# Kernel optimization log

Hardware: AMD Instinct MI355X
Metric: run time of the kernel (lower is better)

## Reference

```python
import jax, jax.numpy as jnp
import numpy as np

V = 32000; D = 1024; H = 16; L = 2; T = 2048; B = 4; C = 32000
DH = D // H
EPS = 1e-5


def layernorm(x, g, b):
    mu = jnp.mean(x, axis=-1, keepdims=True)
    var = jnp.mean((x - mu) ** 2, axis=-1, keepdims=True)
    return (x - mu) * jax.lax.rsqrt(var + EPS) * g + b


def setup_inputs() -> dict:
    key = jax.random.key(0)
    ks = jax.random.split(key, 16)
    s = 0.02
    return {
        "tokens": jax.random.randint(ks[0], (B, T), 0, V),
        "embed_W": jax.random.normal(ks[1], (V, D), jnp.float32) * s,
        "pos_W": jax.random.normal(ks[2], (T, D), jnp.float32) * s,
        "ln_g": jnp.ones((L, D), jnp.float32),
        "ln_b": jnp.zeros((L, D), jnp.float32),
        "qkv_W": jax.random.normal(ks[3], (L, D, 3 * D), jnp.float32) * s,
        "qkv_b": jnp.zeros((L, 3 * D), jnp.float32),
        "out_W": jax.random.normal(ks[4], (L, D, D), jnp.float32) * s,
        "out_b": jnp.zeros((L, D), jnp.float32),
        "lnf_g": jnp.ones((D,), jnp.float32),
        "lnf_b": jnp.zeros((D,), jnp.float32),
        "head_W": jax.random.normal(ks[5], (D, C), jnp.float32) * s,
        "head_b": jnp.zeros((C,), jnp.float32),
    }


def attn_block(x, g, b, Wqkv, bqkv, Wo, bo):
    # pre-LN attention + residual. NOTE: original module defines an MLP but never calls it.
    h = layernorm(x, g, b)
    qkv = h @ Wqkv + bqkv                      # [B,T,3D]
    q, k, v = jnp.split(qkv, 3, axis=-1)
    q = q.reshape(B, T, H, DH)
    k = k.reshape(B, T, H, DH)
    v = v.reshape(B, T, H, DH)
    scores = jnp.einsum("bqhd,bkhd->bhqk", q, k) / np.sqrt(DH)
    causal = jnp.tril(jnp.ones((T, T), bool))
    scores = jnp.where(causal, scores, -jnp.inf)
    attn = jax.nn.softmax(scores, axis=-1)
    o = jnp.einsum("bhqk,bkhd->bqhd", attn, v).reshape(B, T, D)
    return x + o @ Wo + bo


def reference(tokens, embed_W, pos_W, ln_g, ln_b, qkv_W, qkv_b, out_W, out_b,
              lnf_g, lnf_b, head_W, head_b):
    h = embed_W[tokens] + pos_W[jnp.arange(T)][None, :, :]   # [B,T,D]
    for i in range(L):
        h = attn_block(h, ln_g[i], ln_b[i], qkv_W[i], qkv_b[i], out_W[i], out_b[i])
    h = layernorm(h, lnf_g, lnf_b)
    logits = h[:, -1] @ head_W + head_b                      # [B,C]
    return logits
```

## Files before the change

### kernel.cpp

```cpp
#include <hip/hip_runtime.h>

typedef __attribute__((ext_vector_type(8))) __bf16 bf16x8;
typedef __attribute__((ext_vector_type(4))) __bf16 bf16x4;
typedef __attribute__((ext_vector_type(4))) float f32x4;
typedef unsigned long long ull;

static constexpr int kB = 4, kT = 2048, kD = 1024, kH = 16;
static constexpr int kC = 32000, kM = 8192, k3D = 3072, kQK = 2048;

#define MFMA16(a, b, c) __builtin_amdgcn_mfma_f32_16x16x32_bf16((a), (b), (c), 0, 0, 0)

__device__ __forceinline__ void gload_lds16(const __bf16* g, __bf16* l) {
  __builtin_amdgcn_global_load_lds(
      (const __attribute__((address_space(1))) unsigned int*)(const void*)g,
      (__attribute__((address_space(3))) unsigned int*)(void*)l, 16, 0, 0);
}

__global__ __launch_bounds__(256) void embed_ln_kernel(const int* __restrict__ tok,
                                                       const float* __restrict__ embW,
                                                       const float* __restrict__ posW,
                                                       const float* __restrict__ g,
                                                       const float* __restrict__ bb,
                                                       float* __restrict__ h,
                                                       __bf16* __restrict__ hn) {
  const int row = blockIdx.x, tid = threadIdx.x;
  const int t = row & (kT - 1);
  const int tk = tok[row];
  const f32x4 e = ((const f32x4*)(embW + (size_t)tk * kD))[tid];
  const f32x4 p = ((const f32x4*)(posW + (size_t)t * kD))[tid];
  const f32x4 xv = e + p;
  ((f32x4*)(h + (size_t)row * kD))[tid] = xv;
  float s  = xv[0] + xv[1] + xv[2] + xv[3];
  float s2 = xv[0]*xv[0] + xv[1]*xv[1] + xv[2]*xv[2] + xv[3]*xv[3];
  #pragma unroll
  for (int off = 1; off < 64; off <<= 1) {
    s  += __shfl_xor(s, off);
    s2 += __shfl_xor(s2, off);
  }
  __shared__ float red[8];
  const int w = tid >> 6;
  if ((tid & 63) == 0) { red[w*2] = s; red[w*2+1] = s2; }
  __syncthreads();
  s  = red[0] + red[2] + red[4] + red[6];
  s2 = red[1] + red[3] + red[5] + red[7];
  const float mu  = s * (1.f / kD);
  const float var = s2 * (1.f / kD) - mu * mu;
  const float rs  = rsqrtf(var + 1e-5f);
  const f32x4 gv = ((const f32x4*)g)[tid];
  const f32x4 bv = ((const f32x4*)bb)[tid];
  bf16x4 o;
  #pragma unroll
  for (int i = 0; i < 4; i++) o[i] = (__bf16)((xv[i] - mu) * rs * gv[i] + bv[i]);
  ((bf16x4*)(hn + (size_t)row * kD))[tid] = o;
}

template <bool BF16OUT>
__global__ __launch_bounds__(256) void ln_kernel(const float* __restrict__ x,
                                                 const float* __restrict__ g,
                                                 const float* __restrict__ bb,
                                                 void* __restrict__ outp) {
  const int row = blockIdx.x, tid = threadIdx.x;
  const f32x4 xv = ((const f32x4*)(x + (size_t)row * kD))[tid];
  float s  = xv[0] + xv[1] + xv[2] + xv[3];
  float s2 = xv[0]*xv[0] + xv[1]*xv[1] + xv[2]*xv[2] + xv[3]*xv[3];
  #pragma unroll
  for (int off = 1; off < 64; off <<= 1) {
    s  += __shfl_xor(s, off);
    s2 += __shfl_xor(s2, off);
  }
  __shared__ float red[8];
  const int w = tid >> 6;
  if ((tid & 63) == 0) { red[w*2] = s; red[w*2+1] = s2; }
  __syncthreads();
  s  = red[0] + red[2] + red[4] + red[6];
  s2 = red[1] + red[3] + red[5] + red[7];
  const float mu  = s * (1.f / kD);
  const float var = s2 * (1.f / kD) - mu * mu;
  const float rs  = rsqrtf(var + 1e-5f);
  const f32x4 gv = ((const f32x4*)g)[tid];
  const f32x4 bv = ((const f32x4*)bb)[tid];
  if constexpr (BF16OUT) {
    bf16x4 o;
    #pragma unroll
    for (int i = 0; i < 4; i++) o[i] = (__bf16)((xv[i] - mu) * rs * gv[i] + bv[i]);
    ((bf16x4*)((__bf16*)outp + (size_t)row * kD))[tid] = o;
  } else {
    f32x4 o;
    #pragma unroll
    for (int i = 0; i < 4; i++) o[i] = (xv[i] - mu) * rs * gv[i] + bv[i];
    ((f32x4*)((float*)outp + (size_t)row * kD))[tid] = o;
  }
}

__global__ __launch_bounds__(256) void transpose_all_kernel(const float* __restrict__ qkv_W,
                                                            const float* __restrict__ out_W,
                                                            __bf16* __restrict__ WqkvT,
                                                            __bf16* __restrict__ WoT) {
  __shared__ float sh[32][33];
  const int bid = blockIdx.x;
  const float* W; __bf16* WT; int N, tile;
  if (bid < 3072)      { W = qkv_W;                   WT = WqkvT;                    N = k3D; tile = bid; }
  else if (bid < 6144) { W = qkv_W + (size_t)kD*k3D;  WT = WqkvT + (size_t)k3D*kD;   N = k3D; tile = bid - 3072; }
  else                 { W = out_W;                   WT = WoT;                      N = kD;  tile = bid - 6144; }
  const int tx = threadIdx.x & 31, ty = threadIdx.x >> 5;
  const int ntile = N >> 5;
  const int c0 = (tile % ntile) << 5;
  const int r0 = (tile / ntile) << 5;
  #pragma unroll
  for (int i = 0; i < 4; i++) {
    const int r = ty + i * 8;
    sh[r][tx] = W[(size_t)(r0 + r) * N + c0 + tx];
  }
  __syncthreads();
  #pragma unroll
  for (int i = 0; i < 4; i++) {
    const int cc = ty + i * 8;
    WT[(size_t)(c0 + cc) * kD + r0 + tx] = (__bf16)sh[tx][cc];
  }
}

template <bool OUT_BF16>
__global__ __launch_bounds__(256) void gemm_bt_kernel(const __bf16* __restrict__ A,
                                                      const __bf16* __restrict__ BT,
                                                      const float* __restrict__ bias,
                                                      const float* resid,
                                                      float* outf,
                                                      __bf16* outb,
                                                      __bf16* vtp,
                                                      int N, int K, int ldc, int vt_c0,
                                                      int bm_mult, int bm_add) {
  __shared__ __bf16 As[128 * 64];
  __shared__ __bf16 Bs[128 * 64];
  const int tid = threadIdx.x;
  const int lane = tid & 63, w = tid >> 6;
  int wg = (int)blockIdx.x;
  const int nwg = gridDim.x;
  wg = (wg & 7) * (nwg >> 3) + (wg >> 3);
  const int nbn = N >> 7;
  const int bm = (wg / nbn) * bm_mult + bm_add;
  const int bn = wg % nbn;
  const int wr = (w >> 1) * 64, wc = (w & 1) * 64;
  const int lrow = lane & 15, lk8 = (lane >> 4) * 8;

  const int srow = lane >> 3;
  const int scol = (lane & 7) * 8;
  const __bf16* gA = A + (size_t)(bm * 128) * K;
  const __bf16* gB = BT + (size_t)(bn * 128) * K;

  f32x4 acc[4][4] = {};

  for (int k0 = 0; k0 < K; k0 += 64) {
    __syncthreads();
    #pragma unroll
    for (int i = 0; i < 4; i++) {
      const int c = w * 4 + i;
      const int row = c * 8 + srow;
      gload_lds16(gA + (size_t)row * K + k0 + scol, As + c * 512);
      gload_lds16(gB + (size_t)row * K + k0 + scol, Bs + c * 512);
    }
    __syncthreads();
    #pragma unroll
    for (int ks = 0; ks < 2; ks++) {
      bf16x8 af[4], bf[4];
      #pragma unroll
      for (int mt = 0; mt < 4; mt++)
        af[mt] = *(const bf16x8*)(As + (wr + mt * 16 + lrow) * 64 + ks * 32 + lk8);
      #pragma unroll
      for (int nt = 0; nt < 4; nt++)
        bf[nt] = *(const bf16x8*)(Bs + (wc + nt * 16 + lrow) * 64 + ks * 32 + lk8);
      __builtin_amdgcn_s_setprio(1);
      #pragma unroll
      for (int mt = 0; mt < 4; mt++)
        #pragma unroll
        for (int nt = 0; nt < 4; nt++)
          acc[mt][nt] = MFMA16(af[mt], bf[nt], acc[mt][nt]);
      __builtin_amdgcn_s_setprio(0);
    }
  }

  #pragma unroll
  for (int mt = 0; mt < 4; mt++) {
    const int row0 = bm * 128 + wr + mt * 16 + (lane >> 4) * 4;
    #pragma unroll
    for (int nt = 0; nt < 4; nt++) {
      const int col = bn * 128 + wc + nt * 16 + lrow;
      const float bsv = bias[col];
      if (vtp && col >= vt_c0) {
        const int vd = col - vt_c0;
        const int bb_ = row0 >> 11, t = row0 & (kT - 1);
        bf16x4 pk;
        #pragma unroll
        for (int r = 0; r < 4; r++) pk[r] = (__bf16)(acc[mt][nt][r] + bsv);
        *(bf16x4*)(vtp + ((size_t)((bb_ << 4) + (vd >> 6)) * 64 + (vd & 63)) * kT + t) = pk;
      } else {
        #pragma unroll
        for (int r = 0; r < 4; r++) {
          const size_t idx = (size_t)(row0 + r) * ldc + col;
          const float v = acc[mt][nt][r] + bsv;
          if constexpr (OUT_BF16) {
            outb[idx] = (__bf16)v;
          } else {
            outf[idx] = v + resid[idx];
          }
        }
      }
    }
  }
}

__global__ __launch_bounds__(256) void flash0_kernel(const __bf16* __restrict__ qkv,
                                                     const __bf16* __restrict__ vtg,
                                                     __bf16* __restrict__ o) {
  constexpr float SC = 0.18033688011112042f;
  __shared__ __bf16 Ks[64 * 64];
  __shared__ __bf16 Vs[64 * 64];
  const int tid = threadIdx.x, lane = tid & 63, w = tid >> 6;
  int wg = (int)blockIdx.x;
  const int nwg = gridDim.x;
  wg = (wg & 7) * (nwg >> 3) + (wg >> 3);
  const int sub = wg & 15, bh = wg >> 4;
  const int b = bh >> 4, hh = bh & 15;
  const int g = lane >> 4, qown = lane & 15;
  const int r8 = lane >> 3;
  const int sslot = (lane & 7) ^ (r8 & 7);
  const int swz = (qown & 7) << 3;
  const size_t row0 = (size_t)b * kT;

  for (int s = 0; s < 2; s++) {
    const int qt = s ? (31 - sub) : sub;

    const __bf16* qrow = qkv + (row0 + qt * 64 + w * 16 + qown) * kQK + hh * 64;
    bf16x8 qf[2];
    #pragma unroll
    for (int ks = 0; ks < 2; ks++) {
      bf16x8 qr = *(const bf16x8*)(qrow + ks * 32 + 8 * g);
      #pragma unroll
      for (int i = 0; i < 8; i++) qf[ks][i] = (__bf16)((float)qr[i] * SC);
    }

    float m_run = -1e30f, l_run = 0.f;
    f32x4 acc[4] = {};

    for (int kt = 0; kt <= qt; kt++) {
      __syncthreads();
      #pragma unroll
      for (int j = 0; j < 2; j++) {
        const int r = w * 16 + j * 8 + r8;
        gload_lds16(qkv + (row0 + kt * 64 + r) * kQK + 1024 + hh * 64 + sslot * 8,
                    Ks + (w * 16 + j * 8) * 64);
        gload_lds16(vtg + ((size_t)bh * 64 + r) * kT + kt * 64 + sslot * 8,
                    Vs + (w * 16 + j * 8) * 64);
      }
      __syncthreads();

      f32x4 sv[4] = {};
      #pragma unroll
      for (int nt = 0; nt < 4; nt++) {
        const int kr = nt * 16 + qown;
        #pragma unroll
        for (int ks = 0; ks < 2; ks++) {
          bf16x8 kf = *(const bf16x8*)(Ks + kr * 64 + ((ks * 32 + 8 * g) ^ swz));
          sv[nt] = MFMA16(kf, qf[ks], sv[nt]);
        }
      }
      if (kt == qt) {
        #pragma unroll
        for (int nt = 0; nt < 4; nt++)
          #pragma unroll
          for (int r = 0; r < 4; r++)
            if (nt * 16 + 4 * g + r > w * 16 + qown) sv[nt][r] = -1e30f;
      }

      float mx = -1e30f;
      #pragma unroll
      for (int nt = 0; nt < 4; nt++)
        #pragma unroll
        for (int r = 0; r < 4; r++) mx = fmaxf(mx, sv[nt][r]);
      mx = fmaxf(mx, __shfl_xor(mx, 16));
      mx = fmaxf(mx, __shfl_xor(mx, 32));

      float ps = 0.f;
      ull quad[4];
      if (__all(mx - m_run <= 8.0f)) {
        #pragma unroll
        for (int nt = 0; nt < 4; nt++) {
          union { bf16x4 v; ull u; } qd;
          #pragma unroll
          for (int r = 0; r < 4; r++) {
            const float p = exp2f(sv[nt][r] - m_run);
            ps += p;
            qd.v[r] = (__bf16)p;
          }
          quad[nt] = qd.u;
        }
        ps += __shfl_xor(ps, 16);
        ps += __shfl_xor(ps, 32);
        l_run += ps;
      } else {
        const float mnew = fmaxf(m_run, mx);
        const float fsc = exp2f(m_run - mnew);
        m_run = mnew;
        #pragma unroll
        for (int nt = 0; nt < 4; nt++) {
          union { bf16x4 v; ull u; } qd;
          #pragma unroll
          for (int r = 0; r < 4; r++) {
            const float p = exp2f(sv[nt][r] - mnew);
            ps += p;
            qd.v[r] = (__bf16)p;
          }
          quad[nt] = qd.u;
        }
        ps += __shfl_xor(ps, 16);
        ps += __shfl_xor(ps, 32);
        l_run = l_run * fsc + ps;
        float fr[4];
        #pragma unroll
        for (int r = 0; r < 4; r++) fr[r] = __shfl(fsc, 20 * g + r);
        #pragma unroll
        for (int nt = 0; nt < 4; nt++)
          #pragma unroll
          for (int r = 0; r < 4; r++) acc[nt][r] *= fr[r];
      }

      bf16x8 pf[2];
      #pragma unroll
      for (int ks = 0; ks < 2; ks++) {
        const int src = (g & 1) * 32 + qown;
        const ull t0 = __shfl(quad[2 * ks],     src);
        const ull t1 = __shfl(quad[2 * ks + 1], src);
        const ull lo = (g & 2) ? t1 : t0;
        const ull t2 = __shfl(quad[2 * ks],     src + 16);
        const ull t3 = __shfl(quad[2 * ks + 1], src + 16);
        const ull hi = (g & 2) ? t3 : t2;
        union { ull u[2]; bf16x8 v; } pk;
        pk.u[0] = lo; pk.u[1] = hi;
        pf[ks] = pk.v;
      }

      #pragma unroll
      for (int nt = 0; nt < 4; nt++) {
        const int vr = nt * 16 + qown;
        #pragma unroll
        for (int ks = 0; ks < 2; ks++) {
          bf16x8 vf = *(const bf16x8*)(Vs + vr * 64 + ((ks * 32 + 8 * g) ^ swz));
          acc[nt] = MFMA16(pf[ks], vf, acc[nt]);
        }
      }
    }

    const float li = 1.f / l_run;
    float lr[4];
    #pragma unroll
    for (int r = 0; r < 4; r++) lr[r] = __shfl(li, 20 * g + r);
    #pragma unroll
    for (int r = 0; r < 4; r++) {
      const int t = qt * 64 + w * 16 + 4 * g + r;
      #pragma unroll
      for (int nt = 0; nt < 4; nt++)
        o[(row0 + t) * kD + hh * 64 + nt * 16 + qown] = (__bf16)(acc[nt][r] * lr[r]);
    }
  }
}

__global__ __launch_bounds__(256) void flash1_kernel(const __bf16* __restrict__ qkv,
                                                     const __bf16* __restrict__ vtg,
                                                     float* __restrict__ part_acc,
                                                     float* __restrict__ part_ml) {
  constexpr float SC = 0.18033688011112042f;
  __shared__ __bf16 Ks[64 * 64];
  __shared__ __bf16 Vs[64 * 64];
  const int tid = threadIdx.x, lane = tid & 63, w = tid >> 6;
  int wg = (int)blockIdx.x;
  const int nwg = gridDim.x;
  wg = (wg & 7) * (nwg >> 3) + (wg >> 3);
  const int sub = wg & 7, bh = wg >> 3;
  const int b = bh >> 4, hh = bh & 15;
  const int g = lane >> 4, qown = lane & 15;
  const int r8 = lane >> 3;
  const int sslot = (lane & 7) ^ (r8 & 7);
  const int swz = (qown & 7) << 3;
  const size_t row0 = (size_t)b * kT;
  const int qt = 31, ktlo = sub * 4, kthi = ktlo + 4;

  const __bf16* qrow = qkv + (row0 + qt * 64 + w * 16 + qown) * kQK + hh * 64;
  bf16x8 qf[2];
  #pragma unroll
  for (int ks = 0; ks < 2; ks++) {
    bf16x8 qr = *(const bf16x8*)(qrow + ks * 32 + 8 * g);
    #pragma unroll
    for (int i = 0; i < 8; i++) qf[ks][i] = (__bf16)((float)qr[i] * SC);
  }

  float m_run = -1e30f, l_run = 0.f;
  f32x4 acc[4] = {};

  for (int kt = ktlo; kt < kthi; kt++) {
    __syncthreads();
    #pragma unroll
    for (int jj = 0; jj < 2; jj++) {
      const int r = w * 16 + jj * 8 + r8;
      gload_lds16(qkv + (row0 + kt * 64 + r) * kQK + 1024 + hh * 64 + sslot * 8,
                  Ks + (w * 16 + jj * 8) * 64);
      gload_lds16(vtg + ((size_t)bh * 64 + r) * kT + kt * 64 + sslot * 8,
                  Vs + (w * 16 + jj * 8) * 64);
    }
    __syncthreads();

    f32x4 sv[4] = {};
    #pragma unroll
    for (int nt = 0; nt < 4; nt++) {
      const int kr = nt * 16 + qown;
      #pragma unroll
      for (int ks = 0; ks < 2; ks++) {
        bf16x8 kf = *(const bf16x8*)(Ks + kr * 64 + ((ks * 32 + 8 * g) ^ swz));
        sv[nt] = MFMA16(kf, qf[ks], sv[nt]);
      }
    }
    if (kt == qt) {
      #pragma unroll
      for (int nt = 0; nt < 4; nt++)
        #pragma unroll
        for (int r = 0; r < 4; r++)
          if (nt * 16 + 4 * g + r > w * 16 + qown) sv[nt][r] = -1e30f;
    }

    float mx = -1e30f;
    #pragma unroll
    for (int nt = 0; nt < 4; nt++)
      #pragma unroll
      for (int r = 0; r < 4; r++) mx = fmaxf(mx, sv[nt][r]);
    mx = fmaxf(mx, __shfl_xor(mx, 16));
    mx = fmaxf(mx, __shfl_xor(mx, 32));

    const float mnew = fmaxf(m_run, mx);
    const float fsc = exp2f(m_run - mnew);
    m_run = mnew;
    float ps = 0.f;
    ull quad[4];
    #pragma unroll
    for (int nt = 0; nt < 4; nt++) {
      union { bf16x4 v; ull u; } qd;
      #pragma unroll
      for (int r = 0; r < 4; r++) {
        const float p = exp2f(sv[nt][r] - mnew);
        ps += p;
        qd.v[r] = (__bf16)p;
      }
      quad[nt] = qd.u;
    }
    ps += __shfl_xor(ps, 16);
    ps += __shfl_xor(ps, 32);
    l_run = l_run * fsc + ps;
    float fr[4];
    #pragma unroll
    for (int r = 0; r < 4; r++) fr[r] = __shfl(fsc, 20 * g + r);
    #pragma unroll
    for (int nt = 0; nt < 4; nt++)
      #pragma unroll
      for (int r = 0; r < 4; r++) acc[nt][r] *= fr[r];

    bf16x8 pf[2];
    #pragma unroll
    for (int ks = 0; ks < 2; ks++) {
      const int src = (g & 1) * 32 + qown;
      const ull t0 = __shfl(quad[2 * ks],     src);
      const ull t1 = __shfl(quad[2 * ks + 1], src);
      const ull lo = (g & 2) ? t1 : t0;
      const ull t2 = __shfl(quad[2 * ks],     src + 16);
      const ull t3 = __shfl(quad[2 * ks + 1], src + 16);
      const ull hi = (g & 2) ? t3 : t2;
      union { ull u[2]; bf16x8 v; } pk;
      pk.u[0] = lo; pk.u[1] = hi;
      pf[ks] = pk.v;
    }

    #pragma unroll
    for (int nt = 0; nt < 4; nt++) {
      const int vr = nt * 16 + qown;
      #pragma unroll
      for (int ks = 0; ks < 2; ks++) {
        bf16x8 vf = *(const bf16x8*)(Vs + vr * 64 + ((ks * 32 + 8 * g) ^ swz));
        acc[nt] = MFMA16(pf[ks], vf, acc[nt]);
      }
    }
  }

  const int tile = bh * 8 + sub;
  #pragma unroll
  for (int r = 0; r < 4; r++) {
    const int rr = w * 16 + 4 * g + r;
    #pragma unroll
    for (int nt = 0; nt < 4; nt++)
      part_acc[(size_t)tile * 4096 + rr * 64 + nt * 16 + qown] = acc[nt][r];
  }
  if (g == 0) {
    part_ml[tile * 128 + w * 16 + qown] = m_run;
    part_ml[tile * 128 + 64 + w * 16 + qown] = l_run;
  }
}

__global__ __launch_bounds__(256) void flash_merge_kernel(const float* __restrict__ part_acc,
                                                          const float* __restrict__ part_ml,
                                                          __bf16* __restrict__ o) {
  const int bh = blockIdx.x, b = bh >> 4, hh = bh & 15;
  for (int e = threadIdx.x; e < 4096; e += 256) {
    const int row = e >> 6, d = e & 63;
    float mstar = -1e30f;
    #pragma unroll
    for (int kc = 0; kc < 8; kc++)
      mstar = fmaxf(mstar, part_ml[(bh * 8 + kc) * 128 + row]);
    float lstar = 0.f, osum = 0.f;
    #pragma unroll
    for (int kc = 0; kc < 8; kc++) {
      const float wgt = exp2f(part_ml[(bh * 8 + kc) * 128 + row] - mstar);
      lstar += wgt * part_ml[(bh * 8 + kc) * 128 + 64 + row];
      osum  += wgt * part_acc[(size_t)(bh * 8 + kc) * 4096 + e];
    }
    o[(size_t)(b * kT + 1984 + row) * kD + hh * 64 + d] = (__bf16)(osum / lstar);
  }
}

__global__ __launch_bounds__(256) void proj_last_kernel(const __bf16* __restrict__ o,
                                                        const float* __restrict__ W,
                                                        const float* __restrict__ bias,
                                                        const float* __restrict__ h,
                                                        float* __restrict__ out4) {
  const int b = blockIdx.y;
  const int j = blockIdx.x * 256 + threadIdx.x;
  __shared__ float ov[kD];
  const __bf16* orow = o + (size_t)(b * kT + kT - 1) * kD;
  for (int i = threadIdx.x; i < kD; i += 256) ov[i] = (float)orow[i];
  __syncthreads();
  float acc = 0.f;
  #pragma unroll 8
  for (int k = 0; k < kD; k++) acc = fmaf(ov[k], W[(size_t)k * kD + j], acc);
  out4[b * kD + j] = h[(size_t)(b * kT + kT - 1) * kD + j] + bias[j] + acc;
}

__global__ __launch_bounds__(256) void head_kernel(const float* __restrict__ hl,
                                                   const float* __restrict__ W,
                                                   const float* __restrict__ hb,
                                                   float* __restrict__ out) {
  const int jj = threadIdx.x & 63, ks = threadIdx.x >> 6;
  const int j = blockIdx.x * 64 + jj;
  __shared__ float sh[kB * kD];
  __shared__ float red[4][kB][64];
  for (int i = threadIdx.x; i < kB * kD; i += 256) sh[i] = hl[i];
  __syncthreads();
  float a[kB] = {};
  const int k0 = ks * 256;
  #pragma unroll 4
  for (int k = k0; k < k0 + 256; k++) {
    const float wv = W[(size_t)k * kC + j];
    #pragma unroll
    for (int bb = 0; bb < kB; bb++) a[bb] = fmaf(sh[bb * kD + k], wv, a[bb]);
  }
  #pragma unroll
  for (int bb = 0; bb < kB; bb++) red[ks][bb][jj] = a[bb];
  __syncthreads();
  if (ks == 0) {
    const float bv = hb[j];
    #pragma unroll
    for (int bb = 0; bb < kB; bb++)
      out[(size_t)bb * kC + j] = red[0][bb][jj] + red[1][bb][jj] + red[2][bb][jj] + red[3][bb][jj] + bv;
  }
}

extern "C" void kernel_launch(void* const* d_in, const int* in_sizes, int n_in,
                              void* d_out, int out_size, void* d_ws, size_t ws_size,
                              hipStream_t stream) {
  const int*   tokens = (const int*)d_in[0];
  const float* embW   = (const float*)d_in[1];
  const float* posW   = (const float*)d_in[2];
  const float* ln_g   = (const float*)d_in[3];
  const float* ln_b   = (const float*)d_in[4];
  const float* qkv_W  = (const float*)d_in[5];
  const float* qkv_b  = (const float*)d_in[6];
  const float* out_W  = (const float*)d_in[7];
  const float* out_b  = (const float*)d_in[8];
  const float* lnf_g  = (const float*)d_in[9];
  const float* lnf_b  = (const float*)d_in[10];
  const float* headW  = (const float*)d_in[11];
  const float* headb  = (const float*)d_in[12];
  float* logits = (float*)d_out;

  char* ws = (char*)d_ws;
  float*  h     = (float*)(ws);
  __bf16* hn    = (__bf16*)(ws + 33554432);
  __bf16* qkv   = (__bf16*)(ws + 50331648);
  __bf16* Vt    = (__bf16*)(ws + 83886080);
  __bf16* ob    = (__bf16*)(ws + 100663296);
  __bf16* WqkvT = (__bf16*)(ws + 117440512);
  __bf16* WoT   = (__bf16*)(ws + 130613248);
  float*  hl4   = (float*)(ws + 132710400);
  float*  hl    = (float*)(ws + 132726784);
  float* part_acc = (float*)(ws + 33554432);
  float* part_ml  = (float*)(ws + 33554432 + 8388608);

  transpose_all_kernel<<<7168, 256, 0, stream>>>(qkv_W, out_W, WqkvT, WoT);
  embed_ln_kernel<<<kM, 256, 0, stream>>>(tokens, embW, posW, ln_g, ln_b, h, hn);

  gemm_bt_kernel<true><<<(kM/128)*(k3D/128), 256, 0, stream>>>(
      hn, WqkvT, qkv_b, nullptr, nullptr, qkv, Vt, k3D, kD, kQK, 2048, 1, 0);
  flash0_kernel<<<kB*kH*16, 256, 0, stream>>>(qkv, Vt, ob);
  gemm_bt_kernel<false><<<(kM/128)*(kD/128), 256, 0, stream>>>(
      ob, WoT, out_b, h, h, nullptr, nullptr, kD, kD, kD, 1 << 30, 1, 0);

  ln_kernel<true><<<kM, 256, 0, stream>>>(h, ln_g + kD, ln_b + kD, hn);
  gemm_bt_kernel<true><<<(kM/128)*(2048/128), 256, 0, stream>>>(
      hn, WqkvT + (size_t)k3D*kD + (size_t)kD*kD, qkv_b + k3D + kD,
      nullptr, nullptr, qkv + 1024, Vt, 2048, kD, kQK, 1024, 1, 0);
  gemm_bt_kernel<true><<<kB*(kD/128), 256, 0, stream>>>(
      hn, WqkvT + (size_t)k3D*kD, qkv_b + k3D,
      nullptr, nullptr, qkv, nullptr, kD, kD, kQK, 1 << 30, 16, 15);
  flash1_kernel<<<kB*kH*8, 256, 0, stream>>>(qkv, Vt, part_acc, part_ml);
  flash_merge_kernel<<<kB*kH, 256, 0, stream>>>(part_acc, part_ml, ob);
  proj_last_kernel<<<dim3(kD/256, kB), 256, 0, stream>>>(ob, out_W + (size_t)kD*kD,
                                                         out_b + kD, h, hl4);

  ln_kernel<false><<<kB, 256, 0, stream>>>(hl4, lnf_g, lnf_b, hl);
  head_kernel<<<500, 256, 0, stream>>>(hl, headW, headb, logits);
}
```

Measured before the change: 483.1 us.

## Fuse small kernels to cut launch count across the pipeline

Merges the weight transpose and embedding+LayerNorm into one prep kernel, and the layer-1 KV and last-tile Q GEMMs into one launch. The flash merge step moves into flash1 as a last-block-done reduction using an atomic counter and thread fences. The final LayerNorm is folded into the head kernel, which each block recomputes redundantly. This trims launch and serialization overhead, at the cost of an extra memset, atomic synchronization and duplicated LayerNorm work per head block.

```diff
diff --git a/kernel.cpp b/kernel.cpp
--- a/kernel.cpp
+++ b/kernel.cpp
@@ -16,42 +16,70 @@
       (__attribute__((address_space(3))) unsigned int*)(void*)l, 16, 0, 0);
 }
 
-__global__ __launch_bounds__(256) void embed_ln_kernel(const int* __restrict__ tok,
-                                                       const float* __restrict__ embW,
-                                                       const float* __restrict__ posW,
-                                                       const float* __restrict__ g,
-                                                       const float* __restrict__ bb,
-                                                       float* __restrict__ h,
-                                                       __bf16* __restrict__ hn) {
-  const int row = blockIdx.x, tid = threadIdx.x;
-  const int t = row & (kT - 1);
-  const int tk = tok[row];
-  const f32x4 e = ((const f32x4*)(embW + (size_t)tk * kD))[tid];
-  const f32x4 p = ((const f32x4*)(posW + (size_t)t * kD))[tid];
-  const f32x4 xv = e + p;
-  ((f32x4*)(h + (size_t)row * kD))[tid] = xv;
-  float s  = xv[0] + xv[1] + xv[2] + xv[3];
-  float s2 = xv[0]*xv[0] + xv[1]*xv[1] + xv[2]*xv[2] + xv[3]*xv[3];
-  #pragma unroll
-  for (int off = 1; off < 64; off <<= 1) {
-    s  += __shfl_xor(s, off);
-    s2 += __shfl_xor(s2, off);
-  }
-  __shared__ float red[8];
-  const int w = tid >> 6;
-  if ((tid & 63) == 0) { red[w*2] = s; red[w*2+1] = s2; }
-  __syncthreads();
-  s  = red[0] + red[2] + red[4] + red[6];
-  s2 = red[1] + red[3] + red[5] + red[7];
-  const float mu  = s * (1.f / kD);
-  const float var = s2 * (1.f / kD) - mu * mu;
-  const float rs  = rsqrtf(var + 1e-5f);
-  const f32x4 gv = ((const f32x4*)g)[tid];
-  const f32x4 bv = ((const f32x4*)bb)[tid];
-  bf16x4 o;
-  #pragma unroll
-  for (int i = 0; i < 4; i++) o[i] = (__bf16)((xv[i] - mu) * rs * gv[i] + bv[i]);
-  ((bf16x4*)(hn + (size_t)row * kD))[tid] = o;
+__global__ __launch_bounds__(256) void prep_kernel(const float* __restrict__ qkv_W,
+                                                   const float* __restrict__ out_W,
+                                                   __bf16* __restrict__ WqkvT,
+                                                   __bf16* __restrict__ WoT,
+                                                   const int* __restrict__ tok,
+                                                   const float* __restrict__ embW,
+                                                   const float* __restrict__ posW,
+                                                   const float* __restrict__ g,
+                                                   const float* __restrict__ bb,
+                                                   float* __restrict__ h,
+                                                   __bf16* __restrict__ hn) {
+  const int bid = blockIdx.x, tid = threadIdx.x;
+  if (bid < 7168) {
+    __shared__ float sh[32][33];
+    const float* W; __bf16* WT; int N, tile;
+    if (bid < 3072)      { W = qkv_W;                  WT = WqkvT;                  N = k3D; tile = bid; }
+    else if (bid < 6144) { W = qkv_W + (size_t)kD*k3D; WT = WqkvT + (size_t)k3D*kD; N = k3D; tile = bid - 3072; }
+    else                 { W = out_W;                  WT = WoT;                    N = kD;  tile = bid - 6144; }
+    const int tx = tid & 31, ty = tid >> 5;
+    const int ntile = N >> 5;
+    const int c0 = (tile % ntile) << 5;
+    const int r0 = (tile / ntile) << 5;
+    #pragma unroll
+    for (int i = 0; i < 4; i++) {
+      const int r = ty + i * 8;
+      sh[r][tx] = W[(size_t)(r0 + r) * N + c0 + tx];
+    }
+    __syncthreads();
+    #pragma unroll
+    for (int i = 0; i < 4; i++) {
+      const int cc = ty + i * 8;
+      WT[(size_t)(c0 + cc) * kD + r0 + tx] = (__bf16)sh[tx][cc];
+    }
+  } else {
+    const int row = bid - 7168;
+    const int t = row & (kT - 1);
+    const int tk = tok[row];
+    const f32x4 e = ((const f32x4*)(embW + (size_t)tk * kD))[tid];
+    const f32x4 p = ((const f32x4*)(posW + (size_t)t * kD))[tid];
+    const f32x4 xv = e + p;
+    ((f32x4*)(h + (size_t)row * kD))[tid] = xv;
+    float s  = xv[0] + xv[1] + xv[2] + xv[3];
+    float s2 = xv[0]*xv[0] + xv[1]*xv[1] + xv[2]*xv[2] + xv[3]*xv[3];
+    #pragma unroll
+    for (int off = 1; off < 64; off <<= 1) {
+      s  += __shfl_xor(s, off);
+      s2 += __shfl_xor(s2, off);
+    }
+    __shared__ float red[8];
+    const int w = tid >> 6;
+    if ((tid & 63) == 0) { red[w*2] = s; red[w*2+1] = s2; }
+    __syncthreads();
+    s  = red[0] + red[2] + red[4] + red[6];
+    s2 = red[1] + red[3] + red[5] + red[7];
+    const float mu  = s * (1.f / kD);
+    const float var = s2 * (1.f / kD) - mu * mu;
+    const float rs  = rsqrtf(var + 1e-5f);
+    const f32x4 gv = ((const f32x4*)g)[tid];
+    const f32x4 bv = ((const f32x4*)bb)[tid];
+    bf16x4 o;
+    #pragma unroll
+    for (int i = 0; i < 4; i++) o[i] = (__bf16)((xv[i] - mu) * rs * gv[i] + bv[i]);
+    ((bf16x4*)(hn + (size_t)row * kD))[tid] = o;
+  }
 }
 
 template <bool BF16OUT>
@@ -92,56 +120,19 @@
   }
 }
 
-__global__ __launch_bounds__(256) void transpose_all_kernel(const float* __restrict__ qkv_W,
-                                                            const float* __restrict__ out_W,
-                                                            __bf16* __restrict__ WqkvT,
-                                                            __bf16* __restrict__ WoT) {
-  __shared__ float sh[32][33];
-  const int bid = blockIdx.x;
-  const float* W; __bf16* WT; int N, tile;
-  if (bid < 3072)      { W = qkv_W;                   WT = WqkvT;                    N = k3D; tile = bid; }
-  else if (bid < 6144) { W = qkv_W + (size_t)kD*k3D;  WT = WqkvT + (size_t)k3D*kD;   N = k3D; tile = bid - 3072; }
-  else                 { W = out_W;                   WT = WoT;                      N = kD;  tile = bid - 6144; }
-  const int tx = threadIdx.x & 31, ty = threadIdx.x >> 5;
-  const int ntile = N >> 5;
-  const int c0 = (tile % ntile) << 5;
-  const int r0 = (tile / ntile) << 5;
-  #pragma unroll
-  for (int i = 0; i < 4; i++) {
-    const int r = ty + i * 8;
-    sh[r][tx] = W[(size_t)(r0 + r) * N + c0 + tx];
-  }
-  __syncthreads();
-  #pragma unroll
-  for (int i = 0; i < 4; i++) {
-    const int cc = ty + i * 8;
-    WT[(size_t)(c0 + cc) * kD + r0 + tx] = (__bf16)sh[tx][cc];
-  }
-}
-
 template <bool OUT_BF16>
-__global__ __launch_bounds__(256) void gemm_bt_kernel(const __bf16* __restrict__ A,
-                                                      const __bf16* __restrict__ BT,
-                                                      const float* __restrict__ bias,
-                                                      const float* resid,
-                                                      float* outf,
-                                                      __bf16* outb,
-                                                      __bf16* vtp,
-                                                      int N, int K, int ldc, int vt_c0,
-                                                      int bm_mult, int bm_add) {
-  __shared__ __bf16 As[128 * 64];
-  __shared__ __bf16 Bs[128 * 64];
+__device__ __forceinline__ void gemm_body(const __bf16* __restrict__ A,
+                                          const __bf16* __restrict__ BT,
+                                          const float* __restrict__ bias,
+                                          const float* resid, float* outf,
+                                          __bf16* outb, __bf16* vtp,
+                                          int K, int ldc, int vt_c0,
+                                          int bm, int bn,
+                                          __bf16* As, __bf16* Bs) {
   const int tid = threadIdx.x;
   const int lane = tid & 63, w = tid >> 6;
-  int wg = (int)blockIdx.x;
-  const int nwg = gridDim.x;
-  wg = (wg & 7) * (nwg >> 3) + (wg >> 3);
-  const int nbn = N >> 7;
-  const int bm = (wg / nbn) * bm_mult + bm_add;
-  const int bn = wg % nbn;
   const int wr = (w >> 1) * 64, wc = (w & 1) * 64;
   const int lrow = lane & 15, lk8 = (lane >> 4) * 8;
-
   const int srow = lane >> 3;
   const int scol = (lane & 7) * 8;
   const __bf16* gA = A + (size_t)(bm * 128) * K;
@@ -205,6 +196,44 @@
         }
       }
     }
+  }
+}
+
+template <bool OUT_BF16>
+__global__ __launch_bounds__(256) void gemm_bt_kernel(const __bf16* __restrict__ A,
+                                                      const __bf16* __restrict__ BT,
+                                                      const float* __restrict__ bias,
+                                                      const float* resid,
+                                                      float* outf, __bf16* outb, __bf16* vtp,
+                                                      int N, int K, int ldc, int vt_c0) {
+  __shared__ __bf16 As[128 * 64];
+  __shared__ __bf16 Bs[128 * 64];
+  int wg = (int)blockIdx.x;
+  const int nwg = gridDim.x;
+  wg = (wg & 7) * (nwg >> 3) + (wg >> 3);
+  const int nbn = N >> 7;
+  gemm_body<OUT_BF16>(A, BT, bias, resid, outf, outb, vtp, K, ldc, vt_c0,
+                      wg / nbn, wg % nbn, As, Bs);
+}
+
+__global__ __launch_bounds__(256) void gemm_l1_kernel(const __bf16* __restrict__ hn,
+                                                      const __bf16* __restrict__ WkvT,
+                                                      const float* __restrict__ bias_kv,
+                                                      const __bf16* __restrict__ WqT,
+                                                      const float* __restrict__ bias_q,
+                                                      __bf16* __restrict__ qkv,
+                                                      __bf16* __restrict__ vtp) {
+  __shared__ __bf16 As[128 * 64];
+  __shared__ __bf16 Bs[128 * 64];
+  int wg = (int)blockIdx.x;
+  if (wg < 1024) {
+    wg = (wg & 7) * 128 + (wg >> 3);
+    gemm_body<true>(hn, WkvT, bias_kv, nullptr, nullptr, qkv + 1024, vtp,
+                    kD, kQK, 1024, wg / 16, wg % 16, As, Bs);
+  } else {
+    wg -= 1024;
+    gemm_body<true>(hn, WqT, bias_q, nullptr, nullptr, qkv, nullptr,
+                    kD, kQK, 1 << 30, (wg >> 3) * 16 + 15, wg & 7, As, Bs);
   }
 }
 
@@ -366,7 +395,9 @@
 __global__ __launch_bounds__(256) void flash1_kernel(const __bf16* __restrict__ qkv,
                                                      const __bf16* __restrict__ vtg,
                                                      float* __restrict__ part_acc,
-                                                     float* __restrict__ part_ml) {
+                                                     float* __restrict__ part_ml,
+                                                     int* __restrict__ cnt,
+                                                     __bf16* __restrict__ o) {
   constexpr float SC = 0.18033688011112042f;
   __shared__ __bf16 Ks[64 * 64];
   __shared__ __bf16 Vs[64 * 64];
@@ -498,26 +529,28 @@
     part_ml[tile * 128 + w * 16 + qown] = m_run;
     part_ml[tile * 128 + 64 + w * 16 + qown] = l_run;
   }
-}
-
-__global__ __launch_bounds__(256) void flash_merge_kernel(const float* __restrict__ part_acc,
-                                                          const float* __restrict__ part_ml,
-                                                          __bf16* __restrict__ o) {
-  const int bh = blockIdx.x, b = bh >> 4, hh = bh & 15;
-  for (int e = threadIdx.x; e < 4096; e += 256) {
-    const int row = e >> 6, d = e & 63;
-    float mstar = -1e30f;
-    #pragma unroll
-    for (int kc = 0; kc < 8; kc++)
-      mstar = fmaxf(mstar, part_ml[(bh * 8 + kc) * 128 + row]);
-    float lstar = 0.f, osum = 0.f;
-    #pragma unroll
-    for (int kc = 0; kc < 8; kc++) {
-      const float wgt = exp2f(part_ml[(bh * 8 + kc) * 128 + row] - mstar);
-      lstar += wgt * part_ml[(bh * 8 + kc) * 128 + 64 + row];
-      osum  += wgt * part_acc[(size_t)(bh * 8 + kc) * 4096 + e];
-    }
-    o[(size_t)(b * kT + 1984 + row) * kD + hh * 64 + d] = (__bf16)(osum / lstar);
+
+  __threadfence();
+  __shared__ int lastflag;
+  if (tid == 0) lastflag = (atomicAdd(&cnt[bh], 1) == 7) ? 1 : 0;
+  __syncthreads();
+  if (lastflag) {
+    __threadfence();
+    for (int e = tid; e < 4096; e += 256) {
+      const int row = e >> 6, d = e & 63;
+      float mstar = -1e30f;
+      #pragma unroll
+      for (int kc = 0; kc < 8; kc++)
+        mstar = fmaxf(mstar, part_ml[(bh * 8 + kc) * 128 + row]);
+      float lstar = 0.f, osum = 0.f;
+      #pragma unroll
+      for (int kc = 0; kc < 8; kc++) {
+        const float wgt = exp2f(part_ml[(bh * 8 + kc) * 128 + row] - mstar);
+        lstar += wgt * part_ml[(bh * 8 + kc) * 128 + 64 + row];
+        osum  += wgt * part_acc[(size_t)(bh * 8 + kc) * 4096 + e];
+      }
+      o[(size_t)(b * kT + 1984 + row) * kD + hh * 64 + d] = (__bf16)(osum / lstar);
+    }
   }
 }
 
@@ -538,32 +571,56 @@
   out4[b * kD + j] = h[(size_t)(b * kT + kT - 1) * kD + j] + bias[j] + acc;
 }
 
-__global__ __launch_bounds__(256) void head_kernel(const float* __restrict__ hl,
+__global__ __launch_bounds__(256) void head_kernel(const float* __restrict__ hl4,
+                                                   const float* __restrict__ g,
+                                                   const float* __restrict__ bb,
                                                    const float* __restrict__ W,
                                                    const float* __restrict__ hb,
                                                    float* __restrict__ out) {
-  const int jj = threadIdx.x & 63, ks = threadIdx.x >> 6;
-  const int j = blockIdx.x * 64 + jj;
   __shared__ float sh[kB * kD];
   __shared__ float red[4][kB][64];
-  for (int i = threadIdx.x; i < kB * kD; i += 256) sh[i] = hl[i];
+  const int tid = threadIdx.x;
+  const int wv = tid >> 6, ln = tid & 63;
+  {
+    const float* row = hl4 + wv * kD;
+    float vals[16];
+    float s = 0.f, s2 = 0.f;
+    #pragma unroll
+    for (int i = 0; i < 16; i++) {
+      const float v = row[i * 64 + ln];
+      vals[i] = v; s += v; s2 += v * v;
+    }
+    #pragma unroll
+    for (int off = 1; off < 64; off <<= 1) {
+      s += __shfl_xor(s, off); s2 += __shfl_xor(s2, off);
+    }
+    const float mu = s * (1.f / kD);
+    const float rs = rsqrtf(s2 * (1.f / kD) - mu * mu + 1e-5f);
+    #pragma unroll
+    for (int i = 0; i < 16; i++) {
+      const int c = i * 64 + ln;
+      sh[wv * kD + c] = (vals[i] - mu) * rs * g[c] + bb[c];
+    }
+  }
   __syncthreads();
+  const int jj = tid & 63, ks = tid >> 6;
+  const int j = blockIdx.x * 64 + jj;
   float a[kB] = {};
   const int k0 = ks * 256;
   #pragma unroll 4
   for (int k = k0; k < k0 + 256; k++) {
-    const float wv = W[(size_t)k * kC + j];
-    #pragma unroll
-    for (int bb = 0; bb < kB; bb++) a[bb] = fmaf(sh[bb * kD + k], wv, a[bb]);
+    const float wvw = W[(size_t)k * kC + j];
+    #pragma unroll
+    for (int b2 = 0; b2 < kB; b2++) a[b2] = fmaf(sh[b2 * kD + k], wvw, a[b2]);
   }
   #pragma unroll
-  for (int bb = 0; bb < kB; bb++) red[ks][bb][jj] = a[bb];
+  for (int b2 = 0; b2 < kB; b2++) red[ks][b2][jj] = a[b2];
   __syncthreads();
   if (ks == 0) {
     const float bv = hb[j];
     #pragma unroll
-    for (int bb = 0; bb < kB; bb++)
-      out[(size_t)bb * kC + j] = red[0][bb][jj] + red[1][bb][jj] + red[2][bb][jj] + red[3][bb][jj] + bv;
+    for (int b2 = 0; b2 < kB; b2++)
+      out[(size_t)b2 * kC + j] = red[0][b2][jj] + red[1][b2][jj] + red[2][b2][jj] + red[3][b2][jj] + bv;
   }
 }
 
@@ -594,31 +651,26 @@
   __bf16* WqkvT = (__bf16*)(ws + 117440512);
   __bf16* WoT   = (__bf16*)(ws + 130613248);
   float*  hl4   = (float*)(ws + 132710400);
-  float*  hl    = (float*)(ws + 132726784);
   float* part_acc = (float*)(ws + 33554432);
   float* part_ml  = (float*)(ws + 33554432 + 8388608);
-
-  transpose_all_kernel<<<7168, 256, 0, stream>>>(qkv_W, out_W, WqkvT, WoT);
-  embed_ln_kernel<<<kM, 256, 0, stream>>>(tokens, embW, posW, ln_g, ln_b, h, hn);
+  int*   cnt      = (int*)(ws + 33554432 + 8388608 + 262144);
+
+  prep_kernel<<<15360, 256, 0, stream>>>(qkv_W, out_W, WqkvT, WoT,
+                                         tokens, embW, posW, ln_g, ln_b, h, hn);
 
   gemm_bt_kernel<true><<<(kM/128)*(k3D/128), 256, 0, stream>>>(
-      hn, WqkvT, qkv_b, nullptr, nullptr, qkv, Vt, k3D, kD, kQK, 2048, 1, 0);
+      hn, WqkvT, qkv_b, nullptr, nullptr, qkv, Vt, k3D, kD, kQK, 2048);
   flash0_kernel<<<kB*kH*16, 256, 0, stream>>>(qkv, Vt, ob);
   gemm_bt_kernel<false><<<(kM/128)*(kD/128), 256, 0, stream>>>(
-      ob, WoT, out_b, h, h, nullptr, nullptr, kD, kD, kD, 1 << 30, 1, 0);
+      ob, WoT, out_b, h, h, nullptr, nullptr, kD, kD, kD, 1 << 30);
 
   ln_kernel<true><<<kM, 256, 0, stream>>>(h, ln_g + kD, ln_b + kD, hn);
-  gemm_bt_kernel<true><<<(kM/128)*(2048/128), 256, 0, stream>>>(
+  gemm_l1_kernel<<<1056, 256, 0, stream>>>(
       hn, WqkvT + (size_t)k3D*kD + (size_t)kD*kD, qkv_b + k3D + kD,
-      nullptr, nullptr, qkv + 1024, Vt, 2048, kD, kQK, 1024, 1, 0);
-  gemm_bt_kernel<true><<<kB*(kD/128), 256, 0, stream>>>(
-      hn, WqkvT + (size_t)k3D*kD, qkv_b + k3D,
-      nullptr, nullptr, qkv, nullptr, kD, kD, kQK, 1 << 30, 16, 15);
-  flash1_kernel<<<kB*kH*8, 256, 0, stream>>>(qkv, Vt, part_acc, part_ml);
-  flash_merge_kernel<<<kB*kH, 256, 0, stream>>>(part_acc, part_ml, ob);
+      WqkvT + (size_t)k3D*kD, qkv_b + k3D, qkv, Vt);
+  hipMemsetAsync(cnt, 0, 64 * sizeof(int), stream);
+  flash1_kernel<<<kB*kH*8, 256, 0, stream>>>(qkv, Vt, part_acc, part_ml, cnt, ob);
   proj_last_kernel<<<dim3(kD/256, kB), 256, 0, stream>>>(ob, out_W + (size_t)kD*kD,
                                                          out_b + kD, h, hl4);
-
-  ln_kernel<false><<<kB, 256, 0, stream>>>(hl4, lnf_g, lnf_b, hl);
-  head_kernel<<<500, 256, 0, stream>>>(hl, headW, headb, logits);
-}
+  head_kernel<<<kC/64, 256, 0, stream>>>(hl4, lnf_g, lnf_b, headW, headb, logits);
+}
```

Result: slower. 525.8 us (+8.8%).
